# Kernel optimization log

Measured on AMD Instinct MI355X. Metric: run time of the kernel, lower is better.

Reference implementation:

```python
import jax, jax.numpy as jnp
import numpy as np

EMBED = 1024
HEADS = 16
B, T = 4, 2048


def setup_inputs() -> dict:
    key = jax.random.key(0)
    k1, k2, k3, k4, k5 = jax.random.split(key, 5)
    s_in = 1.0 / np.sqrt(EMBED)
    return {
        "x": jax.random.normal(k1, (B, T, EMBED), dtype=jnp.float32),
        "w_qkv": jax.random.uniform(k2, (3 * EMBED, EMBED), jnp.float32, -s_in, s_in),
        "b_qkv": jax.random.uniform(k3, (3 * EMBED,), jnp.float32, -s_in, s_in),
        "w_proj": jax.random.uniform(k4, (EMBED, EMBED), jnp.float32, -s_in, s_in),
        "b_proj": jax.random.uniform(k5, (EMBED,), jnp.float32, -s_in, s_in),
    }


def reference(x, w_qkv, b_qkv, w_proj, b_proj):
    Bz, Tz, C = x.shape
    nh = HEADS
    hs = C // nh
    qkv = jnp.einsum('btc,oc->bto', x, w_qkv) + b_qkv  # [B,T,3C]
    q, k, v = jnp.split(qkv, 3, axis=-1)
    # [B, nh, T, hs]
    q = q.reshape(Bz, Tz, nh, hs).transpose(0, 2, 1, 3)
    k = k.reshape(Bz, Tz, nh, hs).transpose(0, 2, 1, 3)
    v = v.reshape(Bz, Tz, nh, hs).transpose(0, 2, 1, 3)
    scale = 1.0 / np.sqrt(hs).astype(np.float32)
    att = jnp.einsum('bhqd,bhkd->bhqk', q, k) * scale
    causal_mask = jnp.tril(jnp.ones((Tz, Tz), dtype=bool))
    att = jnp.where(causal_mask[None, None], att, jnp.finfo(att.dtype).min)
    att = jax.nn.softmax(att, axis=-1)
    y = jnp.einsum('bhqk,bhkd->bhqd', att, v)
    y = y.transpose(0, 2, 1, 3).reshape(Bz, Tz, C)
    return jnp.einsum('btc,oc->bto', y, w_proj) + b_proj
```

## Files before the change

### kernel.cpp

```cpp
#include <hip/hip_runtime.h>

typedef __bf16 bf16x8 __attribute__((ext_vector_type(8)));
typedef float f32x4 __attribute__((ext_vector_type(4)));

#define DI __device__ __forceinline__

#define WAIT_VMCNT(N)                                        \
  do {                                                       \
    __builtin_amdgcn_sched_barrier(0);                       \
    asm volatile("s_waitcnt vmcnt(" #N ")" ::: "memory");    \
    __builtin_amdgcn_sched_barrier(0);                       \
  } while (0)

DI unsigned short f2bf(float f) {
  unsigned int u = __float_as_uint(f);
  u += 0x7FFFu + ((u >> 16) & 1u);
  return (unsigned short)(u >> 16);
}

DI unsigned cvt_pk_bf16(float a, float b) {
  unsigned r;
  asm("v_cvt_pk_bf16_f32 %0, %1, %2" : "=v"(r) : "v"(a), "v"(b));
  return r;
}

DI float exp2_fast(float x) {
  float r;
  asm("v_exp_f32 %0, %1" : "=v"(r) : "v"(x));
  return r;
}

DI void fence() { asm volatile("" ::: "memory"); }
DI void bar() { fence(); __builtin_amdgcn_s_barrier(); fence(); }

DI bf16x8 ld16(const void* p) {
  union { uint4 u; bf16x8 b; } c;
  c.u = *reinterpret_cast<const uint4*>(p);
  return c.b;
}

DI f32x4 mfma16(bf16x8 a, bf16x8 b, f32x4 c) {
  return __builtin_amdgcn_mfma_f32_16x16x32_bf16(a, b, c, 0, 0, 0);
}

DI void gload_lds16(const void* g, void* l) {
  __builtin_amdgcn_global_load_lds(
      (const __attribute__((address_space(1))) unsigned int*)g,
      (__attribute__((address_space(3))) unsigned int*)l, 16, 0, 0);
}

__global__ void cvt_all(const float* __restrict__ x, const float* __restrict__ wq,
                        const float* __restrict__ wp,
                        unsigned short* __restrict__ xb, unsigned short* __restrict__ wqb,
                        unsigned short* __restrict__ wpb) {
  int i = blockIdx.x * blockDim.x + threadIdx.x;
  const float* s;
  unsigned short* d;
  int off;
  if (i < 2097152) { s = x; d = xb; off = i; }
  else if (i < 2097152 + 786432) { s = wq; d = wqb; off = i - 2097152; }
  else { s = wp; d = wpb; off = i - (2097152 + 786432); }
  float4 v = reinterpret_cast<const float4*>(s)[off];
  uint2 o;
  o.x = cvt_pk_bf16(v.x, v.y);
  o.y = cvt_pk_bf16(v.z, v.w);
  reinterpret_cast<uint2*>(d)[off] = o;
}

template <int N, int MODE>
__global__ __launch_bounds__(256)
void gemm_bt(const unsigned short* __restrict__ A,
             const unsigned short* __restrict__ W,
             const float* __restrict__ bias,
             float* __restrict__ out,
             unsigned short* __restrict__ qo,
             unsigned short* __restrict__ ko,
             unsigned short* __restrict__ vo) {
  constexpr int K = 1024;
  __shared__ __align__(16) char smem[32768];
  char* Asm = smem;
  char* Bsm = smem + 16384;
  const int tid = threadIdx.x;
  const int ln = tid & 63;
  const int w  = tid >> 6;
  const int wm = w >> 1, wn = w & 1;
  const int g = ln >> 4, q = ln & 15;
  const int m0 = blockIdx.x * 128;
  const int n0 = blockIdx.y * 128;

  f32x4 acc[4][4] = {};

  for (int kt = 0; kt < K / 64; ++kt) {
    if (kt) bar();
#pragma unroll
    for (int i = 0; i < 4; ++i) {
      const int chunk = i * 4 + w;
      const int o = chunk * 1024 + ln * 16;
      const int row = o >> 7;
      const int colb = (o & 127) ^ ((row & 7) << 4);
      gload_lds16((const char*)A + ((size_t)(m0 + row) * K + kt * 64) * 2 + colb,
                  Asm + chunk * 1024);
      gload_lds16((const char*)W + ((size_t)(n0 + row) * K + kt * 64) * 2 + colb,
                  Bsm + chunk * 1024);
    }
    WAIT_VMCNT(0);
    bar();
#pragma unroll
    for (int ks = 0; ks < 2; ++ks) {
      bf16x8 av[4], bv[4];
#pragma unroll
      for (int mf = 0; mf < 4; ++mf) {
        const int row = wm * 64 + mf * 16 + q;
        av[mf] = ld16(Asm + ((row * 128 + ks * 64 + g * 16) ^ ((row & 7) << 4)));
      }
#pragma unroll
      for (int nf = 0; nf < 4; ++nf) {
        const int row = wn * 64 + nf * 16 + q;
        bv[nf] = ld16(Bsm + ((row * 128 + ks * 64 + g * 16) ^ ((row & 7) << 4)));
      }
#pragma unroll
      for (int mf = 0; mf < 4; ++mf)
#pragma unroll
        for (int nf = 0; nf < 4; ++nf)
          acc[mf][nf] = mfma16(av[mf], bv[nf], acc[mf][nf]);
    }
  }

#pragma unroll
  for (int nf = 0; nf < 4; ++nf) {
    const int col = n0 + wn * 64 + nf * 16 + q;
    const float bv = bias[col];
#pragma unroll
    for (int mf = 0; mf < 4; ++mf) {
      const int rbase = m0 + wm * 64 + mf * 16 + g * 4;
      if constexpr (MODE == 0) {
#pragma unroll
        for (int r = 0; r < 4; ++r)
          out[(size_t)(rbase + r) * N + col] = acc[mf][nf][r] + bv;
      } else {
        const int b = rbase >> 11, t0 = rbase & 2047;
        if (col < 1024) {
          const int h = col >> 6, d = col & 63;
          unsigned short* qp = qo + ((((size_t)b * 16 + h) << 11) + t0) * 64 + d;
#pragma unroll
          for (int r = 0; r < 4; ++r)
            qp[r * 64] = f2bf((acc[mf][nf][r] + bv) * 0.18033688011112042f);
        } else if (col < 2048) {
          const int c = col - 1024;
          const int h = c >> 6, d = c & 63;
          unsigned short* kp = ko + ((((size_t)b * 16 + h) << 11) + t0) * 64 + d;
#pragma unroll
          for (int r = 0; r < 4; ++r)
            kp[r * 64] = f2bf(acc[mf][nf][r] + bv);
        } else {
          const int c = col - 2048;
          const int h = c >> 6, d = c & 63;
          uint2 pk;
          pk.x = cvt_pk_bf16(acc[mf][nf][0] + bv, acc[mf][nf][1] + bv);
          pk.y = cvt_pk_bf16(acc[mf][nf][2] + bv, acc[mf][nf][3] + bv);
          *(uint2*)(vo + ((((size_t)b * 16 + h) << 6) + d) * 2048 + t0) = pk;
        }
      }
    }
  }
}

__global__ __launch_bounds__(256)
void attn_fwd(const unsigned short* __restrict__ Qb,
              const unsigned short* __restrict__ Kb,
              const unsigned short* __restrict__ Vtb,
              unsigned short* __restrict__ Yb) {
  __shared__ __align__(16) char smem[32768];
  char* Psm = smem + 16384;
  const int tid = threadIdx.x;
  const int ln = tid & 63;
  const int w = tid >> 6;
  const int g = ln >> 4, q = ln & 15;
  const int bh = blockIdx.x;
  __constant__ static const int QMAP[16] = {15, 14, 13, 12, 8, 9, 10, 11,
                                            4, 5, 6, 7, 3, 2, 1, 0};
  const int qt = QMAP[blockIdx.y];
  const size_t base = (size_t)bh * 2048 * 64;
  const int b = bh >> 4, h = bh & 15;
  const int q0 = qt * 128;
  const int qw = q0 + w * 32;

  auto stage = [&](int j) {
    const int kv0 = j << 6;
    const char* Kg = (const char*)(Kb + base + (size_t)kv0 * 64);
    const char* Vg = (const char*)(Vtb + base) + kv0 * 2;
#pragma unroll
    for (int i = 0; i < 2; ++i) {
      const int chunk = i * 4 + w;
      const int o = chunk * 1024 + ln * 16;
      const int row = o >> 7;
      const int colb = (o & 127) ^ ((row & 7) << 4);
      gload_lds16(Kg + row * 128 + colb, smem + chunk * 1024);
      gload_lds16(Vg + (size_t)row * 4096 + colb, smem + 8192 + chunk * 1024);
    }
  };

  bf16x8 qf[2][2];
#pragma unroll
  for (int nf = 0; nf < 2; ++nf)
#pragma unroll
    for (int kf = 0; kf < 2; ++kf)
      qf[nf][kf] = ld16(Qb + base + (size_t)(qw + nf * 16 + q) * 64 + kf * 32 + g * 8);

  float m_run[2] = {-INFINITY, -INFINITY};
  float l_run[2] = {0.f, 0.f};
  f32x4 yt[4][2] = {};

  const int nkv = (q0 >> 6) + 2;
  for (int j = 0; j < nkv; ++j) {
    stage(j);
    WAIT_VMCNT(0);
    bar();

    const int kv0 = j << 6;
    const char* Ksm = smem;
    const char* Vsm = smem + 8192;
    const bool active = (kv0 <= qw + 31);
    if (active) {
      f32x4 st[4][2] = {};
      __builtin_amdgcn_s_setprio(1);
#pragma unroll
      for (int mf = 0; mf < 4; ++mf) {
        const int row = mf * 16 + q;
        const int swz = (row & 7) << 4;
        const bf16x8 a0 = ld16(Ksm + ((row * 128 + g * 16) ^ swz));
        const bf16x8 a1 = ld16(Ksm + ((row * 128 + 64 + g * 16) ^ swz));
#pragma unroll
        for (int nf = 0; nf < 2; ++nf) {
          st[mf][nf] = mfma16(a0, qf[nf][0], st[mf][nf]);
          st[mf][nf] = mfma16(a1, qf[nf][1], st[mf][nf]);
        }
      }
      __builtin_amdgcn_s_setprio(0);
      if (kv0 + 63 > qw) {
#pragma unroll
        for (int mf = 0; mf < 4; ++mf)
#pragma unroll
          for (int nf = 0; nf < 2; ++nf)
#pragma unroll
            for (int r = 0; r < 4; ++r)
              if (kv0 + mf * 16 + g * 4 + r > qw + nf * 16 + q)
                st[mf][nf][r] = -INFINITY;
      }
#pragma unroll
      for (int nf = 0; nf < 2; ++nf) {
        float vmax = -INFINITY;
#pragma unroll
        for (int mf = 0; mf < 4; ++mf) {
          const f32x4 v = st[mf][nf];
          vmax = fmaxf(fmaxf(vmax, fmaxf(v[0], v[1])), fmaxf(v[2], v[3]));
        }
        vmax = fmaxf(vmax, __shfl_xor(vmax, 16));
        vmax = fmaxf(vmax, __shfl_xor(vmax, 32));
        const float mo = m_run[nf];
        if (__any(vmax > mo)) {
          const float mn = fmaxf(mo, vmax);
          const float corr = exp2_fast(mo - mn);
          m_run[nf] = mn;
          l_run[nf] *= corr;
#pragma unroll
          for (int mfd = 0; mfd < 4; ++mfd) yt[mfd][nf] *= corr;
        }
        const float mcur = m_run[nf];
        float ls = 0.f;
#pragma unroll
        for (int mf = 0; mf < 4; ++mf) {
          f32x4 p;
#pragma unroll
          for (int r = 0; r < 4; ++r) p[r] = exp2_fast(st[mf][nf][r] - mcur);
          ls += (p[0] + p[1]) + (p[2] + p[3]);
          uint2 pk2;
          pk2.x = cvt_pk_bf16(p[0], p[1]);
          pk2.y = cvt_pk_bf16(p[2], p[3]);
          const int prow = w * 32 + nf * 16 + q;
          *(uint2*)(Psm + ((prow * 128 + mf * 32 + g * 8) ^ ((prow & 7) << 4))) = pk2;
        }
        ls += __shfl_xor(ls, 16);
        ls += __shfl_xor(ls, 32);
        l_run[nf] += ls;
      }
      __builtin_amdgcn_s_setprio(1);
#pragma unroll
      for (int kf = 0; kf < 2; ++kf) {
        bf16x8 pb[2];
#pragma unroll
        for (int nf = 0; nf < 2; ++nf) {
          const int prow = w * 32 + nf * 16 + q;
          pb[nf] = ld16(Psm + ((prow * 128 + kf * 64 + g * 16) ^ ((prow & 7) << 4)));
        }
#pragma unroll
        for (int mfd = 0; mfd < 4; ++mfd) {
          const int vrow = mfd * 16 + q;
          const bf16x8 vv = ld16(Vsm + ((vrow * 128 + kf * 64 + g * 16) ^ ((vrow & 7) << 4)));
#pragma unroll
          for (int nf = 0; nf < 2; ++nf)
            yt[mfd][nf] = mfma16(vv, pb[nf], yt[mfd][nf]);
        }
      }
      __builtin_amdgcn_s_setprio(0);
    }
    bar();
  }

#pragma unroll
  for (int nf = 0; nf < 2; ++nf) {
    const float inv = 1.f / l_run[nf];
    const int qr = qw + nf * 16 + q;
    unsigned short* yp = Yb + (size_t)(b * 2048 + qr) * 1024 + h * 64;
#pragma unroll
    for (int mfd = 0; mfd < 4; ++mfd) {
      uint2 o2;
      o2.x = cvt_pk_bf16(yt[mfd][nf][0] * inv, yt[mfd][nf][1] * inv);
      o2.y = cvt_pk_bf16(yt[mfd][nf][2] * inv, yt[mfd][nf][3] * inv);
      *(uint2*)(yp + mfd * 16 + g * 4) = o2;
    }
  }
}

extern "C" void kernel_launch(void* const* d_in, const int* in_sizes, int n_in,
                              void* d_out, int out_size, void* d_ws, size_t ws_size,
                              hipStream_t stream) {
  const float* x      = (const float*)d_in[0];
  const float* w_qkv  = (const float*)d_in[1];
  const float* b_qkv  = (const float*)d_in[2];
  const float* w_proj = (const float*)d_in[3];
  const float* b_proj = (const float*)d_in[4];
  float* out = (float*)d_out;
  char* ws = (char*)d_ws;

  unsigned short* xb  = (unsigned short*)(ws);
  unsigned short* wqb = (unsigned short*)(ws + (size_t)(16 << 20));
  unsigned short* wpb = (unsigned short*)(ws + (size_t)(22 << 20));
  unsigned short* Qb  = (unsigned short*)(ws + (size_t)(24 << 20));
  unsigned short* Kb  = (unsigned short*)(ws + (size_t)(40 << 20));
  unsigned short* Vtb = (unsigned short*)(ws + (size_t)(56 << 20));
  unsigned short* Yb  = (unsigned short*)(ws + (size_t)(72 << 20));

  cvt_all<<<12288, 256, 0, stream>>>(x, w_qkv, w_proj, xb, wqb, wpb);
  gemm_bt<3072, 1><<<dim3(64, 24), 256, 0, stream>>>(xb, wqb, b_qkv, nullptr, Qb, Kb, Vtb);
  attn_fwd<<<dim3(64, 16), 256, 0, stream>>>(Qb, Kb, Vtb, Yb);
  gemm_bt<1024, 0><<<dim3(64, 8), 256, 0, stream>>>(Yb, wpb, b_proj, out, nullptr, nullptr, nullptr);
}
```

Baseline: 178.9 us.

## Load K/V fragments directly from global memory, drop shared staging and barriers

```diff
diff --git a/kernel.cpp b/kernel.cpp
--- a/kernel.cpp
+++ b/kernel.cpp
@@ -165,40 +165,24 @@
   }
 }
 
-__global__ __launch_bounds__(256)
+__global__ __launch_bounds__(256, 3)
 void attn_fwd(const unsigned short* __restrict__ Qb,
               const unsigned short* __restrict__ Kb,
               const unsigned short* __restrict__ Vtb,
               unsigned short* __restrict__ Yb) {
-  __shared__ __align__(16) char smem[32768];
-  char* Psm = smem + 16384;
+  __shared__ __align__(16) char smem[16384];
   const int tid = threadIdx.x;
   const int ln = tid & 63;
   const int w = tid >> 6;
   const int g = ln >> 4, q = ln & 15;
+  char* Psm = smem + w * 4096;
   const int bh = blockIdx.x;
   __constant__ static const int QMAP[16] = {15, 14, 13, 12, 8, 9, 10, 11,
                                             4, 5, 6, 7, 3, 2, 1, 0};
   const int qt = QMAP[blockIdx.y];
   const size_t base = (size_t)bh * 2048 * 64;
   const int b = bh >> 4, h = bh & 15;
-  const int q0 = qt * 128;
-  const int qw = q0 + w * 32;
-
-  auto stage = [&](int j) {
-    const int kv0 = j << 6;
-    const char* Kg = (const char*)(Kb + base + (size_t)kv0 * 64);
-    const char* Vg = (const char*)(Vtb + base) + kv0 * 2;
-#pragma unroll
-    for (int i = 0; i < 2; ++i) {
-      const int chunk = i * 4 + w;
-      const int o = chunk * 1024 + ln * 16;
-      const int row = o >> 7;
-      const int colb = (o & 127) ^ ((row & 7) << 4);
-      gload_lds16(Kg + row * 128 + colb, smem + chunk * 1024);
-      gload_lds16(Vg + (size_t)row * 4096 + colb, smem + 8192 + chunk * 1024);
-    }
-  };
+  const int qw = qt * 128 + w * 32;
 
   bf16x8 qf[2][2];
 #pragma unroll
@@ -211,100 +195,93 @@
   float l_run[2] = {0.f, 0.f};
   f32x4 yt[4][2] = {};
 
-  const int nkv = (q0 >> 6) + 2;
+  const char* Kl = (const char*)(Kb + base + (size_t)q * 64) + g * 16;
+  const char* Vl = (const char*)(Vtb + base + (size_t)q * 2048) + g * 16;
+
+  const int nkv = ((qw + 31) >> 6) + 1;
   for (int j = 0; j < nkv; ++j) {
-    stage(j);
-    WAIT_VMCNT(0);
-    bar();
-
     const int kv0 = j << 6;
-    const char* Ksm = smem;
-    const char* Vsm = smem + 8192;
-    const bool active = (kv0 <= qw + 31);
-    if (active) {
-      f32x4 st[4][2] = {};
-      __builtin_amdgcn_s_setprio(1);
+    f32x4 st[4][2] = {};
+    __builtin_amdgcn_s_setprio(1);
+#pragma unroll
+    for (int mf = 0; mf < 4; ++mf) {
+      const char* kp = Kl + (size_t)(kv0 + mf * 16) * 128;
+      const bf16x8 a0 = ld16(kp);
+      const bf16x8 a1 = ld16(kp + 64);
+#pragma unroll
+      for (int nf = 0; nf < 2; ++nf) {
+        st[mf][nf] = mfma16(a0, qf[nf][0], st[mf][nf]);
+        st[mf][nf] = mfma16(a1, qf[nf][1], st[mf][nf]);
+      }
+    }
+    __builtin_amdgcn_s_setprio(0);
+    if (kv0 + 63 > qw) {
+#pragma unroll
+      for (int mf = 0; mf < 4; ++mf)
+#pragma unroll
+        for (int nf = 0; nf < 2; ++nf)
+#pragma unroll
+          for (int r = 0; r < 4; ++r)
+            if (kv0 + mf * 16 + g * 4 + r > qw + nf * 16 + q)
+              st[mf][nf][r] = -INFINITY;
+    }
+#pragma unroll
+    for (int nf = 0; nf < 2; ++nf) {
+      float vmax = -INFINITY;
 #pragma unroll
       for (int mf = 0; mf < 4; ++mf) {
-        const int row = mf * 16 + q;
-        const int swz = (row & 7) << 4;
-        const bf16x8 a0 = ld16(Ksm + ((row * 128 + g * 16) ^ swz));
-        const bf16x8 a1 = ld16(Ksm + ((row * 128 + 64 + g * 16) ^ swz));
-#pragma unroll
-        for (int nf = 0; nf < 2; ++nf) {
-          st[mf][nf] = mfma16(a0, qf[nf][0], st[mf][nf]);
-          st[mf][nf] = mfma16(a1, qf[nf][1], st[mf][nf]);
-        }
-      }
-      __builtin_amdgcn_s_setprio(0);
-      if (kv0 + 63 > qw) {
-#pragma unroll
-        for (int mf = 0; mf < 4; ++mf)
-#pragma unroll
-          for (int nf = 0; nf < 2; ++nf)
-#pragma unroll
-            for (int r = 0; r < 4; ++r)
-              if (kv0 + mf * 16 + g * 4 + r > qw + nf * 16 + q)
-                st[mf][nf][r] = -INFINITY;
-      }
+        const f32x4 v = st[mf][nf];
+        vmax = fmaxf(fmaxf(vmax, fmaxf(v[0], v[1])), fmaxf(v[2], v[3]));
+      }
+      vmax = fmaxf(vmax, __shfl_xor(vmax, 16));
+      vmax = fmaxf(vmax, __shfl_xor(vmax, 32));
+      const float mo = m_run[nf];
+      if (__any(vmax > mo)) {
+        const float mn = fmaxf(mo, vmax);
+        const float corr = exp2_fast(mo - mn);
+        m_run[nf] = mn;
+        l_run[nf] *= corr;
+#pragma unroll
+        for (int mfd = 0; mfd < 4; ++mfd) yt[mfd][nf] *= corr;
+      }
+      const float mcur = m_run[nf];
+      float ls = 0.f;
+#pragma unroll
+      for (int mf = 0; mf < 4; ++mf) {
+        f32x4 p;
+#pragma unroll
+        for (int r = 0; r < 4; ++r) p[r] = exp2_fast(st[mf][nf][r] - mcur);
+        ls += (p[0] + p[1]) + (p[2] + p[3]);
+        uint2 pk2;
+        pk2.x = cvt_pk_bf16(p[0], p[1]);
+        pk2.y = cvt_pk_bf16(p[2], p[3]);
+        const int prow = nf * 16 + q;
+        *(uint2*)(Psm + ((prow * 128 + mf * 32 + g * 8) ^ ((prow & 7) << 4))) = pk2;
+      }
+      ls += __shfl_xor(ls, 16);
+      ls += __shfl_xor(ls, 32);
+      l_run[nf] += ls;
+    }
+    asm volatile("s_waitcnt lgkmcnt(0)" ::: "memory");
+    __builtin_amdgcn_sched_barrier(0);
+    __builtin_amdgcn_s_setprio(1);
+#pragma unroll
+    for (int kf = 0; kf < 2; ++kf) {
+      bf16x8 pb[2];
 #pragma unroll
       for (int nf = 0; nf < 2; ++nf) {
-        float vmax = -INFINITY;
-#pragma unroll
-        for (int mf = 0; mf < 4; ++mf) {
-          const f32x4 v = st[mf][nf];
-          vmax = fmaxf(fmaxf(vmax, fmaxf(v[0], v[1])), fmaxf(v[2], v[3]));
-        }
-        vmax = fmaxf(vmax, __shfl_xor(vmax, 16));
-        vmax = fmaxf(vmax, __shfl_xor(vmax, 32));
-        const float mo = m_run[nf];
-        if (__any(vmax > mo)) {
-          const float mn = fmaxf(mo, vmax);
-          const float corr = exp2_fast(mo - mn);
-          m_run[nf] = mn;
-          l_run[nf] *= corr;
-#pragma unroll
-          for (int mfd = 0; mfd < 4; ++mfd) yt[mfd][nf] *= corr;
-        }
-        const float mcur = m_run[nf];
-        float ls = 0.f;
-#pragma unroll
-        for (int mf = 0; mf < 4; ++mf) {
-          f32x4 p;
-#pragma unroll
-          for (int r = 0; r < 4; ++r) p[r] = exp2_fast(st[mf][nf][r] - mcur);
-          ls += (p[0] + p[1]) + (p[2] + p[3]);
-          uint2 pk2;
-          pk2.x = cvt_pk_bf16(p[0], p[1]);
-          pk2.y = cvt_pk_bf16(p[2], p[3]);
-          const int prow = w * 32 + nf * 16 + q;
-          *(uint2*)(Psm + ((prow * 128 + mf * 32 + g * 8) ^ ((prow & 7) << 4))) = pk2;
-        }
-        ls += __shfl_xor(ls, 16);
-        ls += __shfl_xor(ls, 32);
-        l_run[nf] += ls;
-      }
-      __builtin_amdgcn_s_setprio(1);
-#pragma unroll
-      for (int kf = 0; kf < 2; ++kf) {
-        bf16x8 pb[2];
-#pragma unroll
-        for (int nf = 0; nf < 2; ++nf) {
-          const int prow = w * 32 + nf * 16 + q;
-          pb[nf] = ld16(Psm + ((prow * 128 + kf * 64 + g * 16) ^ ((prow & 7) << 4)));
-        }
-#pragma unroll
-        for (int mfd = 0; mfd < 4; ++mfd) {
-          const int vrow = mfd * 16 + q;
-          const bf16x8 vv = ld16(Vsm + ((vrow * 128 + kf * 64 + g * 16) ^ ((vrow & 7) << 4)));
-#pragma unroll
-          for (int nf = 0; nf < 2; ++nf)
-            yt[mfd][nf] = mfma16(vv, pb[nf], yt[mfd][nf]);
-        }
-      }
-      __builtin_amdgcn_s_setprio(0);
-    }
-    bar();
+        const int prow = nf * 16 + q;
+        pb[nf] = ld16(Psm + ((prow * 128 + kf * 64 + g * 16) ^ ((prow & 7) << 4)));
+      }
+#pragma unroll
+      for (int mfd = 0; mfd < 4; ++mfd) {
+        const bf16x8 vv = ld16(Vl + (size_t)(mfd * 16) * 4096 + kv0 * 2 + kf * 64);
+#pragma unroll
+        for (int nf = 0; nf < 2; ++nf)
+          yt[mfd][nf] = mfma16(vv, pb[nf], yt[mfd][nf]);
+      }
+    }
+    __builtin_amdgcn_s_setprio(0);
   }
 
 #pragma unroll
```

After: 230.2 us. +28.7%, slower.
